# Performance work log

Hardware: AMD Instinct MI355X
Metric: run time of the kernel (lower is better)

Reference implementation:

```python
import jax, jax.numpy as jnp
import numpy as np

B, S, N, D, QD = 32, 256, 50, 100, 768


def _xavier(key, fan_out, fan_in):
    lim = float(np.sqrt(6.0 / (fan_in + fan_out)))
    return jax.random.uniform(key, (fan_out, fan_in), jnp.float32, -lim, lim)


def setup_inputs() -> dict:
    key = jax.random.key(0)
    ks = jax.random.split(key, 8)
    q = jax.random.normal(ks[0], (B, QD), jnp.float32)
    k = jax.random.normal(ks[1], (B, S, N, D), jnp.float32)
    v = jax.random.normal(ks[2], (B, S, N, D), jnp.float32)
    input_ent = jax.random.randint(ks[3], (B, S), 0, 100000)
    Q_w = _xavier(ks[4], D, QD)
    V_w = _xavier(ks[5], D, D)
    bq = 1.0 / np.sqrt(QD)
    bv = 1.0 / np.sqrt(D)
    Q_b = jax.random.uniform(ks[6], (D,), jnp.float32, -bq, bq)
    V_b = jax.random.uniform(ks[7], (D,), jnp.float32, -bv, bv)
    return {"input_ent": input_ent, "q": q, "k": k, "v": v,
            "Q_w": Q_w, "Q_b": Q_b, "V_w": V_w, "V_b": V_b}


def reference(input_ent, q, k, v, Q_w, Q_b, V_w, V_b):
    # Q projection + L2 normalize over feature dim (F.normalize eps=1e-12)
    Q = q @ Q_w.T + Q_b                                            # [B, D]
    Qn = Q / jnp.maximum(jnp.linalg.norm(Q, axis=1, keepdims=True), 1e-12)
    # Keys/values share the same V_linear projection of v (k arg unused, as in source)
    K = jnp.einsum('bsnd,ed->bsne', v, V_w) + V_b                  # [B, S, N, D]
    # detached L2 norm with zero->1e-6 replacement
    l2 = jax.lax.stop_gradient(jnp.linalg.norm(K, axis=3, keepdims=True))
    l2 = jnp.where(l2 == 0.0, 1e-6, l2)
    Kn = K / l2
    # cosine-similarity scores over neighbors
    att = jnp.einsum('bd,bsnd->bsn', Qn, Kn)                       # [B, S, N]
    att = jnp.where(att == 0.0, -10000.0, att)
    att = jax.nn.softmax(jax.nn.leaky_relu(att, 0.01), axis=2)
    # zero out positions where softmax was exactly uniform (pad rows)
    att = jnp.where(att == 1.0 / att.shape[-1], 0.0, att)
    # weighted sum of values (V_linear(v) == K)
    out = jnp.einsum('bsn,bsnd->bsd', att, K)                      # [B, S, D]
    # mode == 'candidate': return combined directly (graphsage=False)
    return out
```

## Files before the change

kernel.cpp:

```cpp
#include <hip/hip_runtime.h>
#include <math.h>


#define S_DIM 256
#define N_NBR 50
#define D_F   100
#define QD    768
#define NT    7
#define KC    4
#define TILE_F4 1250
#define ITERS 16

typedef __attribute__((ext_vector_type(4))) float f32x4;
typedef __attribute__((ext_vector_type(8))) short s16x8;
typedef __attribute__((ext_vector_type(4))) short s16x4;

__device__ __forceinline__ short f2bf(float f) {
  union { float f; unsigned u; } x; x.f = f;
  unsigned r = x.u + 0x7fffu + ((x.u >> 16) & 1u);
  return (short)(r >> 16);
}

__global__ __launch_bounds__(256, 2) void wga_kernel(
    const float* __restrict__ v, const float* __restrict__ q,
    const float* __restrict__ Qw, const float* __restrict__ Qb,
    const float* __restrict__ Vw, const float* __restrict__ Vb,
    float* __restrict__ out) {
  __shared__ __align__(16) short Abuf[KC * 4 * 64 * 8];
  __shared__ float Kl[N_NBR + 2][105];
  __shared__ __align__(16) float attS[64];
  __shared__ float QnS[112];
  __shared__ float nrm2[64], srw[64];
  __shared__ float qs[QD];
  __shared__ float Qpart[256];
  __shared__ float rnS;

  const int t  = threadIdx.x;
  const int w  = t >> 6, l = t & 63;
  const int qd = l >> 4, m = l & 15;
  const int blk = blockIdx.x;
  const int b   = blk >> 4;
  const int s0  = (blk & 15) * ITERS;

  f32x4 pf[5];
  {
    const f32x4* vt = (const f32x4*)(v + (size_t)(b * S_DIM + s0) * (N_NBR * D_F));
#pragma unroll
    for (int j = 0; j < 5; ++j) {
      const int i = t + 256 * j;
      if (i < TILE_F4) pf[j] = vt[i];
    }
  }

  s16x8 bfrag[NT][KC];
  float bias[NT], QnSv[NT];
#pragma unroll
  for (int nt = 0; nt < NT; ++nt) {
    const int e = nt * 16 + m;
    bias[nt] = (e < D_F) ? Vb[e] : 0.f;
#pragma unroll
    for (int c = 0; c < KC; ++c) {
      const int k0 = c * 32 + qd * 8;
      s16x8 pk;
#pragma unroll
      for (int j = 0; j < 8; ++j) {
        const int k = k0 + j;
        const float x = (e < D_F && k < D_F) ? Vw[e * D_F + k] : 0.f;
        pk[j] = f2bf(x);
      }
      bfrag[nt][c] = pk;
    }
  }

  {
    int4* az = (int4*)Abuf;
    for (int i = t; i < 1024; i += 256) az[i] = make_int4(0, 0, 0, 0);
    float* klz = &Kl[N_NBR][0];
    if (t < 210) klz[t] = 0.f;
    for (int i = t; i < QD; i += 256) qs[i] = q[b * QD + i];
  }
  __syncthreads();

  if (t < 200) {
    const int e = t >> 1, h = t & 1;
    const float4* wr = (const float4*)(Qw + e * QD + h * 384);
    const float4* qv = (const float4*)(qs + h * 384);
    float a0 = 0.f, a1 = 0.f, a2 = 0.f, a3 = 0.f;
#pragma unroll 4
    for (int f = 0; f < 96; ++f) {
      float4 wv = wr[f], qf = qv[f];
      a0 += wv.x * qf.x; a1 += wv.y * qf.y; a2 += wv.z * qf.z; a3 += wv.w * qf.w;
    }
    Qpart[t] = (a0 + a1) + (a2 + a3);
  }
  __syncthreads();
  if (t < D_F)       QnS[t] = Qpart[2 * t] + Qpart[2 * t + 1] + Qb[t];
  else if (t < 112)  QnS[t] = 0.f;
  __syncthreads();
  if (w == 0) {
    float x = QnS[l] * QnS[l];
    if (l < 48) x += QnS[64 + l] * QnS[64 + l];
#pragma unroll
    for (int d = 1; d < 64; d <<= 1) x += __shfl_xor(x, d, 64);
    if (l == 0) rnS = 1.0f / fmaxf(sqrtf(x), 1e-12f);
  }
  __syncthreads();
  if (t < D_F) QnS[t] *= rnS;
  __syncthreads();
#pragma unroll
  for (int nt = 0; nt < NT; ++nt) QnSv[nt] = QnS[nt * 16 + m];

  for (int it = 0; it < ITERS; ++it) {
#pragma unroll
    for (int j = 0; j < 5; ++j) {
      const int i = t + 256 * j;
      if (i < TILE_F4) {
        const int n  = i / 25;
        const int k4 = (i - n * 25) * 4;
        const int wv = n >> 4, mm = n & 15;
        const int c = k4 >> 5, qq = (k4 >> 3) & 3, j0 = k4 & 7;
        s16x4 p;
        p[0] = f2bf(pf[j][0]); p[1] = f2bf(pf[j][1]);
        p[2] = f2bf(pf[j][2]); p[3] = f2bf(pf[j][3]);
        *(s16x4*)&Abuf[(((c * 4 + wv) * 64 + qq * 16 + mm) << 3) + j0] = p;
      }
    }
    __syncthreads();

    if (it + 1 < ITERS) {
      const f32x4* vt = (const f32x4*)(v + (size_t)(b * S_DIM + s0 + it + 1) * (N_NBR * D_F));
#pragma unroll
      for (int j = 0; j < 5; ++j) {
        const int i = t + 256 * j;
        if (i < TILE_F4) pf[j] = vt[i];
      }
    }

    f32x4 acc[NT];
#pragma unroll
    for (int nt = 0; nt < NT; ++nt) {
      f32x4 z; z[0] = bias[nt]; z[1] = bias[nt]; z[2] = bias[nt]; z[3] = bias[nt];
      acc[nt] = z;
    }
    s16x8 af[KC];
#pragma unroll
    for (int c = 0; c < KC; ++c)
      af[c] = *(const s16x8*)&Abuf[((c * 4 + w) * 64 + l) * 8];
#pragma unroll
    for (int c = 0; c < KC; ++c)
#pragma unroll
      for (int nt = 0; nt < NT; ++nt)
        acc[nt] = __builtin_amdgcn_mfma_f32_16x16x32_bf16(af[c], bfrag[nt][c], acc[nt], 0, 0, 0);

#pragma unroll
    for (int r = 0; r < 4; ++r) {
      float np = 0.f, sp = 0.f;
#pragma unroll
      for (int nt = 0; nt < NT; ++nt) {
        const float kv = acc[nt][r];
        np += kv * kv;
        sp += QnSv[nt] * kv;
      }
#pragma unroll
      for (int d = 1; d < 16; d <<= 1) {
        np += __shfl_xor(np, d, 64);
        sp += __shfl_xor(sp, d, 64);
      }
      if (m == 0) {
        const int row = w * 16 + qd * 4 + r;
        nrm2[row] = np; srw[row] = sp;
      }
    }
#pragma unroll
    for (int nt = 0; nt < NT; ++nt) {
      const int col = nt * 16 + m;
#pragma unroll
      for (int r = 0; r < 4; ++r) {
        const int row = w * 16 + qd * 4 + r;
        if (row < N_NBR && col < D_F) Kl[row][col] = acc[nt][r];
      }
    }
    __syncthreads();

    if (w == 0) {
      float a = -1e30f;
      if (l < N_NBR) {
        float l2 = sqrtf(nrm2[l]);
        if (l2 == 0.f) l2 = 1e-6f;
        float sc = srw[l] / l2;
        if (sc == 0.f) sc = -10000.f;
        a = (sc >= 0.f) ? sc : 0.01f * sc;
      }
      float mx = a;
#pragma unroll
      for (int d = 1; d < 64; d <<= 1) mx = fmaxf(mx, __shfl_xor(mx, d, 64));
      const float e = (l < N_NBR) ? __expf(a - mx) : 0.f;
      float sm = e;
#pragma unroll
      for (int d = 1; d < 64; d <<= 1) sm += __shfl_xor(sm, d, 64);
      float att = e / sm;
      if (att == 0.02f) att = 0.f;
      attS[l] = (l < N_NBR) ? att : 0.f;
    }
    __syncthreads();

    if (t < D_F) {
      float o = 0.f;
#pragma unroll
      for (int c = 0; c < 13; ++c) {
        float4 av = *(const float4*)&attS[c * 4];
        o += av.x * Kl[c * 4 + 0][t];
        o += av.y * Kl[c * 4 + 1][t];
        o += av.z * Kl[c * 4 + 2][t];
        o += av.w * Kl[c * 4 + 3][t];
      }
      out[(size_t)(b * S_DIM + s0 + it) * D_F + t] = o;
    }
  }
}

extern "C" void kernel_launch(void* const* d_in, const int* in_sizes, int n_in,
                              void* d_out, int out_size, void* d_ws, size_t ws_size,
                              hipStream_t stream) {
  const float* q  = (const float*)d_in[1];
  const float* v  = (const float*)d_in[3];
  const float* Qw = (const float*)d_in[4];
  const float* Qb = (const float*)d_in[5];
  const float* Vw = (const float*)d_in[6];
  const float* Vb = (const float*)d_in[7];
  float* out = (float*)d_out;
  (void)d_ws; (void)ws_size;

  wga_kernel<<<512, 256, 0, stream>>>(v, q, Qw, Qb, Vw, Vb, out);
}
```

Measured before the change: 346.2 us.

## Assign one sequence position per wavefront and drop block-wide barriers in main loop

Each wavefront now processes a whole (b,s) tile of 50 neighbors on its own. It loads v rows straight from global memory into MFMA A fragments, keeps all four M-tiles of accumulators in registers, and does the softmax and weighted sum inside the wave using shuffles. The V_w B-fragments move from registers to shared memory. This removes the per-iteration __syncthreads, the LDS staging of A and K, and the prefetch pipeline. In exchange, register pressure rises sharply (4x7 accumulators plus 16 A fragments), global loads are no longer prefetched, and occupancy may fall.

```diff
diff --git a/kernel.cpp b/kernel.cpp
--- a/kernel.cpp
+++ b/kernel.cpp
@@ -8,12 +8,9 @@
 #define QD    768
 #define NT    7
 #define KC    4
-#define TILE_F4 1250
-#define ITERS 16
 
 typedef __attribute__((ext_vector_type(4))) float f32x4;
 typedef __attribute__((ext_vector_type(8))) short s16x8;
-typedef __attribute__((ext_vector_type(4))) short s16x4;
 
 __device__ __forceinline__ short f2bf(float f) {
   union { float f; unsigned u; } x; x.f = f;
@@ -26,58 +23,41 @@
     const float* __restrict__ Qw, const float* __restrict__ Qb,
     const float* __restrict__ Vw, const float* __restrict__ Vb,
     float* __restrict__ out) {
-  __shared__ __align__(16) short Abuf[KC * 4 * 64 * 8];
-  __shared__ float Kl[N_NBR + 2][105];
-  __shared__ __align__(16) float attS[64];
-  __shared__ float QnS[112];
-  __shared__ float nrm2[64], srw[64];
+  __shared__ __align__(16) short BlS[28 * 64 * 8];
   __shared__ float qs[QD];
   __shared__ float Qpart[256];
+  __shared__ float QnS[112];
   __shared__ float rnS;
+  __shared__ float nrm2W[4][64], srwW[4][64], attW[4][64];
 
   const int t  = threadIdx.x;
   const int w  = t >> 6, l = t & 63;
   const int qd = l >> 4, m = l & 15;
   const int blk = blockIdx.x;
   const int b   = blk >> 4;
-  const int s0  = (blk & 15) * ITERS;
-
-  f32x4 pf[5];
-  {
-    const f32x4* vt = (const f32x4*)(v + (size_t)(b * S_DIM + s0) * (N_NBR * D_F));
-#pragma unroll
-    for (int j = 0; j < 5; ++j) {
-      const int i = t + 256 * j;
-      if (i < TILE_F4) pf[j] = vt[i];
-    }
-  }
-
-  s16x8 bfrag[NT][KC];
-  float bias[NT], QnSv[NT];
-#pragma unroll
-  for (int nt = 0; nt < NT; ++nt) {
-    const int e = nt * 16 + m;
-    bias[nt] = (e < D_F) ? Vb[e] : 0.f;
-#pragma unroll
-    for (int c = 0; c < KC; ++c) {
-      const int k0 = c * 32 + qd * 8;
-      s16x8 pk;
+  const int s0  = (blk & 15) << 4;
+
+  for (int i = t; i < QD; i += 256) qs[i] = q[b * QD + i];
+
+  for (int idx = t; idx < 28 * 64; idx += 256) {
+    const int g  = idx >> 6, ll = idx & 63;
+    const int c  = g / 7, nt = g - 7 * c;
+    const int col = nt * 16 + (ll & 15);
+    const int k0  = c * 32 + (ll >> 4) * 8;
+    s16x8 pk;
+    if (c < 3 && col < D_F) {
+      const f32x4 u0 = *(const f32x4*)(Vw + col * D_F + k0);
+      const f32x4 u1 = *(const f32x4*)(Vw + col * D_F + k0 + 4);
+#pragma unroll
+      for (int j = 0; j < 4; ++j) { pk[j] = f2bf(u0[j]); pk[4 + j] = f2bf(u1[j]); }
+    } else {
 #pragma unroll
       for (int j = 0; j < 8; ++j) {
         const int k = k0 + j;
-        const float x = (e < D_F && k < D_F) ? Vw[e * D_F + k] : 0.f;
-        pk[j] = f2bf(x);
-      }
-      bfrag[nt][c] = pk;
-    }
-  }
-
-  {
-    int4* az = (int4*)Abuf;
-    for (int i = t; i < 1024; i += 256) az[i] = make_int4(0, 0, 0, 0);
-    float* klz = &Kl[N_NBR][0];
-    if (t < 210) klz[t] = 0.f;
-    for (int i = t; i < QD; i += 256) qs[i] = q[b * QD + i];
+        pk[j] = f2bf((col < D_F && k < D_F) ? Vw[col * D_F + k] : 0.f);
+      }
+    }
+    *(s16x8*)&BlS[idx * 8] = pk;
   }
   __syncthreads();
 
@@ -107,87 +87,98 @@
   __syncthreads();
   if (t < D_F) QnS[t] *= rnS;
   __syncthreads();
-#pragma unroll
-  for (int nt = 0; nt < NT; ++nt) QnSv[nt] = QnS[nt * 16 + m];
-
-  for (int it = 0; it < ITERS; ++it) {
-#pragma unroll
-    for (int j = 0; j < 5; ++j) {
-      const int i = t + 256 * j;
-      if (i < TILE_F4) {
-        const int n  = i / 25;
-        const int k4 = (i - n * 25) * 4;
-        const int wv = n >> 4, mm = n & 15;
-        const int c = k4 >> 5, qq = (k4 >> 3) & 3, j0 = k4 & 7;
-        s16x4 p;
-        p[0] = f2bf(pf[j][0]); p[1] = f2bf(pf[j][1]);
-        p[2] = f2bf(pf[j][2]); p[3] = f2bf(pf[j][3]);
-        *(s16x4*)&Abuf[(((c * 4 + wv) * 64 + qq * 16 + mm) << 3) + j0] = p;
-      }
-    }
-    __syncthreads();
-
-    if (it + 1 < ITERS) {
-      const f32x4* vt = (const f32x4*)(v + (size_t)(b * S_DIM + s0 + it + 1) * (N_NBR * D_F));
-#pragma unroll
-      for (int j = 0; j < 5; ++j) {
-        const int i = t + 256 * j;
-        if (i < TILE_F4) pf[j] = vt[i];
-      }
-    }
-
-    f32x4 acc[NT];
-#pragma unroll
-    for (int nt = 0; nt < NT; ++nt) {
-      f32x4 z; z[0] = bias[nt]; z[1] = bias[nt]; z[2] = bias[nt]; z[3] = bias[nt];
-      acc[nt] = z;
-    }
-    s16x8 af[KC];
-#pragma unroll
-    for (int c = 0; c < KC; ++c)
-      af[c] = *(const s16x8*)&Abuf[((c * 4 + w) * 64 + l) * 8];
-#pragma unroll
-    for (int c = 0; c < KC; ++c)
+
+  float QnSv[NT], bias[NT];
+#pragma unroll
+  for (int nt = 0; nt < NT; ++nt) {
+    const int col = nt * 16 + m;
+    QnSv[nt] = QnS[col];
+    bias[nt] = (col < D_F) ? Vb[col] : 0.f;
+  }
+
+  for (int tt = 0; tt < 4; ++tt) {
+    const int s = s0 + (tt << 2) + w;
+    const float* vb = v + (size_t)(b * S_DIM + s) * (N_NBR * D_F);
+
+    s16x8 afr[4][KC];
+#pragma unroll
+    for (int hp = 0; hp < 2; ++hp) {
+      f32x4 L[2][KC], H[2][KC];
+#pragma unroll
+      for (int i = 0; i < 2; ++i) {
+        const int mt  = hp * 2 + i;
+        const int row = mt * 16 + m;
+        const bool rv = row < N_NBR;
+        const float* ap = vb + row * D_F;
+#pragma unroll
+        for (int c = 0; c < KC; ++c) {
+          const int k0 = c * 32 + qd * 8;
+          f32x4 z = {0.f, 0.f, 0.f, 0.f};
+          L[i][c] = z; H[i][c] = z;
+          if (rv && k0 <= 96) L[i][c] = *(const f32x4*)(ap + k0);
+          if (rv && k0 <= 92) H[i][c] = *(const f32x4*)(ap + k0 + 4);
+        }
+      }
+#pragma unroll
+      for (int i = 0; i < 2; ++i)
+#pragma unroll
+        for (int c = 0; c < KC; ++c) {
+          s16x8 pa;
+#pragma unroll
+          for (int j = 0; j < 4; ++j) { pa[j] = f2bf(L[i][c][j]); pa[4 + j] = f2bf(H[i][c][j]); }
+          afr[hp * 2 + i][c] = pa;
+        }
+    }
+
+    f32x4 acc[4][NT];
+#pragma unroll
+    for (int mt = 0; mt < 4; ++mt)
+#pragma unroll
+      for (int nt = 0; nt < NT; ++nt) {
+        f32x4 bz; bz[0] = bias[nt]; bz[1] = bias[nt]; bz[2] = bias[nt]; bz[3] = bias[nt];
+        acc[mt][nt] = bz;
+      }
+#pragma unroll
+    for (int c = 0; c < KC; ++c) {
+      s16x8 bf[NT];
 #pragma unroll
       for (int nt = 0; nt < NT; ++nt)
-        acc[nt] = __builtin_amdgcn_mfma_f32_16x16x32_bf16(af[c], bfrag[nt][c], acc[nt], 0, 0, 0);
-
-#pragma unroll
-    for (int r = 0; r < 4; ++r) {
-      float np = 0.f, sp = 0.f;
-#pragma unroll
-      for (int nt = 0; nt < NT; ++nt) {
-        const float kv = acc[nt][r];
-        np += kv * kv;
-        sp += QnSv[nt] * kv;
-      }
-#pragma unroll
-      for (int d = 1; d < 16; d <<= 1) {
-        np += __shfl_xor(np, d, 64);
-        sp += __shfl_xor(sp, d, 64);
-      }
-      if (m == 0) {
-        const int row = w * 16 + qd * 4 + r;
-        nrm2[row] = np; srw[row] = sp;
-      }
-    }
-#pragma unroll
-    for (int nt = 0; nt < NT; ++nt) {
-      const int col = nt * 16 + m;
+        bf[nt] = *(const s16x8*)&BlS[(((c * 7 + nt) << 6) + l) * 8];
+#pragma unroll
+      for (int mt = 0; mt < 4; ++mt)
+#pragma unroll
+        for (int nt = 0; nt < NT; ++nt)
+          acc[mt][nt] = __builtin_amdgcn_mfma_f32_16x16x32_bf16(afr[mt][c], bf[nt], acc[mt][nt], 0, 0, 0);
+    }
+
+#pragma unroll
+    for (int mt = 0; mt < 4; ++mt)
 #pragma unroll
       for (int r = 0; r < 4; ++r) {
-        const int row = w * 16 + qd * 4 + r;
-        if (row < N_NBR && col < D_F) Kl[row][col] = acc[nt][r];
-      }
-    }
-    __syncthreads();
-
-    if (w == 0) {
+        float np = 0.f, sp = 0.f;
+#pragma unroll
+        for (int nt = 0; nt < NT; ++nt) {
+          const float kv = acc[mt][nt][r];
+          np += kv * kv;
+          sp += QnSv[nt] * kv;
+        }
+#pragma unroll
+        for (int d = 1; d < 16; d <<= 1) {
+          np += __shfl_xor(np, d, 64);
+          sp += __shfl_xor(sp, d, 64);
+        }
+        if (m == 0) {
+          const int row = mt * 16 + qd * 4 + r;
+          nrm2W[w][row] = np; srwW[w][row] = sp;
+        }
+      }
+
+    {
       float a = -1e30f;
       if (l < N_NBR) {
-        float l2 = sqrtf(nrm2[l]);
+        float l2 = sqrtf(nrm2W[w][l]);
         if (l2 == 0.f) l2 = 1e-6f;
-        float sc = srw[l] / l2;
+        float sc = srwW[w][l] / l2;
         if (sc == 0.f) sc = -10000.f;
         a = (sc >= 0.f) ? sc : 0.01f * sc;
       }
@@ -200,22 +191,34 @@
       for (int d = 1; d < 64; d <<= 1) sm += __shfl_xor(sm, d, 64);
       float att = e / sm;
       if (att == 0.02f) att = 0.f;
-      attS[l] = (l < N_NBR) ? att : 0.f;
-    }
-    __syncthreads();
-
-    if (t < D_F) {
-      float o = 0.f;
-#pragma unroll
-      for (int c = 0; c < 13; ++c) {
-        float4 av = *(const float4*)&attS[c * 4];
-        o += av.x * Kl[c * 4 + 0][t];
-        o += av.y * Kl[c * 4 + 1][t];
-        o += av.z * Kl[c * 4 + 2][t];
-        o += av.w * Kl[c * 4 + 3][t];
-      }
-      out[(size_t)(b * S_DIM + s0 + it) * D_F + t] = o;
-    }
+      attW[w][l] = (l < N_NBR) ? att : 0.f;
+    }
+
+    float ar[4][4];
+#pragma unroll
+    for (int mt = 0; mt < 4; ++mt)
+#pragma unroll
+      for (int r = 0; r < 4; ++r)
+        ar[mt][r] = attW[w][mt * 16 + qd * 4 + r];
+
+    float o[NT];
+#pragma unroll
+    for (int nt = 0; nt < NT; ++nt) {
+      float ov = 0.f;
+#pragma unroll
+      for (int mt = 0; mt < 4; ++mt)
+#pragma unroll
+        for (int r = 0; r < 4; ++r)
+          ov = fmaf(ar[mt][r], acc[mt][nt][r], ov);
+      ov += __shfl_xor(ov, 16, 64);
+      ov += __shfl_xor(ov, 32, 64);
+      o[nt] = ov;
+    }
+    const float slo = (qd == 0) ? o[0] : (qd == 1) ? o[1] : (qd == 2) ? o[2] : o[3];
+    const float shi = (qd == 0) ? o[4] : (qd == 1) ? o[5] : o[6];
+    float* op = out + (size_t)(b * S_DIM + s) * D_F;
+    op[l] = slo;
+    if (l < 36) op[64 + l] = shi;
   }
 }
 
```

Result: slower. 398.6 us (+15.1%).
